# Kernel tuning notes

Measured on AMD Instinct MI355X. Metric: run time of the kernel, lower is better.

## Reference

```python
import jax, jax.numpy as jnp
import numpy as np

B, T, H, LD = 32, 2048, 1024, 1024

def setup_inputs() -> dict:
    key = jax.random.key(0)
    k1, k2, k3, k4, k5 = jax.random.split(key, 5)
    scale = 1.0 / np.sqrt(H)
    return {
        "encoder_hidden": jax.random.normal(k1, (B, T, H), dtype=jnp.float32),
        "decoder_hidden": jax.random.normal(k2, (B, H), dtype=jnp.float32),
        "W1": jax.random.normal(k3, (H, LD), dtype=jnp.float32) * scale,
        "b1": jnp.zeros((LD,), dtype=jnp.float32),
        "W2": jax.random.normal(k4, (H, LD), dtype=jnp.float32) * scale,
        "b2": jnp.zeros((LD,), dtype=jnp.float32),
        "V": jax.random.normal(k5, (LD, 1), dtype=jnp.float32) * (1.0 / np.sqrt(LD)),
        "bV": jnp.zeros((1,), dtype=jnp.float32),
    }

def reference(encoder_hidden, decoder_hidden, W1, b1, W2, b2, V, bV):
    # dec proj: [B, 1, ld]
    dec_w = (decoder_hidden @ W1 + b1)[:, None, :]
    # enc proj: [B, T, ld]
    enc_w = jnp.einsum('bth,hl->btl', encoder_hidden, W2) + b2
    # multiplicative combine (as in source: decoder_Weight * encoder_weight)
    score = jnp.tanh(dec_w * enc_w) @ V + bV          # [B, T, 1]
    attn = jax.nn.softmax(score, axis=1)              # softmax over time
    context = jnp.sum(attn * encoder_hidden, axis=1)  # [B, H]
    return context, attn
```

## Files before the change

kernel.cpp:

```cpp
#include <hip/hip_runtime.h>
#include <hip/hip_bf16.h>
#include <math.h>

#define B_  32
#define T_  2048
#define H_  1024
#define LD_ 1024
#define M_  (B_*T_)

typedef __attribute__((ext_vector_type(8))) short bf16x8;
typedef __attribute__((ext_vector_type(4))) float f32x4;

__device__ __forceinline__ void async_copy16(void* lds, const void* g) {
  __builtin_amdgcn_global_load_lds(
      (const __attribute__((address_space(1))) void*)g,
      (__attribute__((address_space(3))) void*)lds, 16, 0, 0);
}

__global__ void convert_w2(const float* __restrict__ W2, __hip_bfloat16* __restrict__ w2p) {
  int idx = blockIdx.x * 256 + threadIdx.x;
  int kg = idx >> 10, n = idx & 1023;
  __align__(16) __hip_bfloat16 h[8];
#pragma unroll
  for (int j = 0; j < 8; ++j)
    h[j] = __float2bfloat16(W2[(size_t)(kg * 8 + j) * LD_ + n]);
  *reinterpret_cast<uint4*>(&w2p[(size_t)kg * (LD_ * 8) + n * 8]) =
      *reinterpret_cast<const uint4*>(h);
}

__global__ void dec_proj(const float* __restrict__ dec, const float* __restrict__ W1,
                         const float* __restrict__ b1, float* __restrict__ dec_w) {
  __shared__ float sdec[H_];
  int bb = blockIdx.x >> 2;
  int l = (blockIdx.x & 3) * 256 + threadIdx.x;
  for (int i = threadIdx.x; i < H_; i += 256) sdec[i] = dec[bb * H_ + i];
  __syncthreads();
  float a0 = 0.f, a1 = 0.f, a2 = 0.f, a3 = 0.f;
  for (int h = 0; h < H_; h += 4) {
    a0 += sdec[h + 0] * W1[(h + 0) * LD_ + l];
    a1 += sdec[h + 1] * W1[(h + 1) * LD_ + l];
    a2 += sdec[h + 2] * W1[(h + 2) * LD_ + l];
    a3 += sdec[h + 3] * W1[(h + 3) * LD_ + l];
  }
  dec_w[bb * LD_ + l] = (a0 + a1) + (a2 + a3) + b1[l];
}

__global__ __launch_bounds__(256, 2)
void score_gemm(const float* __restrict__ enc,
                const __hip_bfloat16* __restrict__ w2p,
                const float* __restrict__ dec_w,
                const float* __restrict__ b2,
                const float* __restrict__ V,
                float* __restrict__ score) {
  __shared__ __align__(16) __hip_bfloat16 Asm[2][4][128][8];
  __shared__ __align__(16) __hip_bfloat16 Bsm[2][4][256][8];

  const int tid  = threadIdx.x;
  const int lane = tid & 63;
  const int wave = tid >> 6;
  const int wm = wave >> 1, wn = wave & 1;
  const int bid = blockIdx.y * gridDim.x + blockIdx.x;
  const int swz = (bid & 7) * 256 + (bid >> 3);
  const int mb = swz >> 2, nb = swz & 3;
  const int row0 = mb * 128, col0 = nb * 256;
  const int q = lane >> 4, c15 = lane & 15;

  f32x4 acc[4][8] = {};

  const int sm  = tid >> 2;
  const int skg = tid & 3;
  const int sx  = skg * 2;

  const size_t arow0 = (size_t)(row0 + sm) * H_ + skg * 8;
  const size_t arow1 = (size_t)(row0 + 64 + sm) * H_ + skg * 8;

  float4 pf[4];

  auto LOADA = [&](int k0) {
    pf[0] = *reinterpret_cast<const float4*>(enc + arow0 + k0);
    pf[1] = *reinterpret_cast<const float4*>(enc + arow0 + k0 + 4);
    pf[2] = *reinterpret_cast<const float4*>(enc + arow1 + k0);
    pf[3] = *reinterpret_cast<const float4*>(enc + arow1 + k0 + 4);
  };
  auto CVTW = [&](int buf) {
    __align__(16) __hip_bfloat16 h[8];
    h[0] = __float2bfloat16(pf[0].x); h[1] = __float2bfloat16(pf[0].y);
    h[2] = __float2bfloat16(pf[0].z); h[3] = __float2bfloat16(pf[0].w);
    h[4] = __float2bfloat16(pf[1].x); h[5] = __float2bfloat16(pf[1].y);
    h[6] = __float2bfloat16(pf[1].z); h[7] = __float2bfloat16(pf[1].w);
    *reinterpret_cast<uint4*>(&Asm[buf][skg][sm ^ sx][0]) =
        *reinterpret_cast<const uint4*>(h);
    h[0] = __float2bfloat16(pf[2].x); h[1] = __float2bfloat16(pf[2].y);
    h[2] = __float2bfloat16(pf[2].z); h[3] = __float2bfloat16(pf[2].w);
    h[4] = __float2bfloat16(pf[3].x); h[5] = __float2bfloat16(pf[3].y);
    h[6] = __float2bfloat16(pf[3].z); h[7] = __float2bfloat16(pf[3].w);
    *reinterpret_cast<uint4*>(&Asm[buf][skg][(64 + sm) ^ sx][0]) =
        *reinterpret_cast<const uint4*>(h);
  };
  auto GLOADB = [&](int buf, int k0) {
    char* bbase = (char*)&Bsm[buf][0][0][0] + tid * 16;
    const char* gbase = (const char*)w2p + ((size_t)(k0 >> 3)) * (LD_ * 8 * 2)
                        + (size_t)col0 * 16 + tid * 16;
#pragma unroll
    for (int p = 0; p < 4; ++p)
      async_copy16(bbase + p * 4096, gbase + (size_t)p * (LD_ * 8 * 2));
  };

  LOADA(0);
  GLOADB(0, 0);
  CVTW(0);
  __syncthreads();

  for (int t = 0; t < 32; ++t) {
    const int cur = t & 1;
    if (t < 31) {
      LOADA((t + 1) * 32);
      GLOADB(cur ^ 1, (t + 1) * 32);
    }
    bf16x8 af[4], bfr[8];
#pragma unroll
    for (int i = 0; i < 4; ++i)
      af[i] = *reinterpret_cast<const bf16x8*>(
          &Asm[cur][q][(wm * 64 + i * 16 + c15) ^ (q * 2)][0]);
#pragma unroll
    for (int j = 0; j < 8; ++j)
      bfr[j] = *reinterpret_cast<const bf16x8*>(
          &Bsm[cur][q][wn * 128 + j * 16 + c15][0]);
#pragma unroll
    for (int i = 0; i < 4; ++i)
#pragma unroll
      for (int j = 0; j < 8; ++j)
        acc[i][j] = __builtin_amdgcn_mfma_f32_16x16x32_bf16(af[i], bfr[j], acc[i][j], 0, 0, 0);
    if (t < 31) CVTW(cur ^ 1);
    __syncthreads();
  }

  const int bb = row0 >> 11;
  float b2v[8], dwv[8], Vv[8];
#pragma unroll
  for (int j = 0; j < 8; ++j) {
    int n = col0 + wn * 128 + j * 16 + c15;
    b2v[j] = b2[n];
    dwv[j] = dec_w[bb * LD_ + n];
    Vv[j]  = V[n];
  }
#pragma unroll
  for (int i = 0; i < 4; ++i) {
#pragma unroll
    for (int r = 0; r < 4; ++r) {
      float v = 0.f;
#pragma unroll
      for (int j = 0; j < 8; ++j) {
        float e = acc[i][j][r] + b2v[j];
        v += tanhf(dwv[j] * e) * Vv[j];
      }
      v += __shfl_xor(v, 1);
      v += __shfl_xor(v, 2);
      v += __shfl_xor(v, 4);
      v += __shfl_xor(v, 8);
      if (c15 == 0) {
        int row = row0 + wm * 64 + i * 16 + q * 4 + r;
        atomicAdd(&score[row], v);
      }
    }
  }
}

__global__ void softmax_k(const float* __restrict__ score, float* __restrict__ attn) {
  int bb = blockIdx.x;
  int tid = threadIdx.x;
  int lane = tid & 63, wave = tid >> 6;
  __shared__ float red[4];
  float v[8];
  float mx = -3.4e38f;
#pragma unroll
  for (int i = 0; i < 8; ++i) {
    v[i] = score[bb * T_ + i * 256 + tid];
    mx = fmaxf(mx, v[i]);
  }
#pragma unroll
  for (int m = 32; m >= 1; m >>= 1) mx = fmaxf(mx, __shfl_xor(mx, m));
  if (lane == 0) red[wave] = mx;
  __syncthreads();
  mx = fmaxf(fmaxf(red[0], red[1]), fmaxf(red[2], red[3]));
  __syncthreads();
  float s = 0.f;
#pragma unroll
  for (int i = 0; i < 8; ++i) { v[i] = __expf(v[i] - mx); s += v[i]; }
#pragma unroll
  for (int m = 32; m >= 1; m >>= 1) s += __shfl_xor(s, m);
  if (lane == 0) red[wave] = s;
  __syncthreads();
  s = red[0] + red[1] + red[2] + red[3];
  float inv = 1.f / s;
#pragma unroll
  for (int i = 0; i < 8; ++i) attn[bb * T_ + i * 256 + tid] = v[i] * inv;
}

__global__ __launch_bounds__(256)
void context_k(const float* __restrict__ enc, const float* __restrict__ attn,
               float* __restrict__ ctx) {
  const int bb = blockIdx.y;
  const int t0 = blockIdx.x * 128;
  __shared__ float sat[128];
  if (threadIdx.x < 128) sat[threadIdx.x] = attn[bb * T_ + t0 + threadIdx.x];
  __syncthreads();
  const float4* base = reinterpret_cast<const float4*>(
      enc + ((size_t)bb * T_ + t0) * H_) + threadIdx.x;
  f32x4 a0 = {}, a1 = {}, a2 = {}, a3 = {};
  for (int t = 0; t < 128; t += 8) {
    float4 v[8];
#pragma unroll
    for (int u = 0; u < 8; ++u) v[u] = base[(size_t)(t + u) * (H_ / 4)];
#pragma unroll
    for (int u = 0; u < 8; ++u) {
      float a = sat[t + u];
      f32x4& d = (u & 2) ? ((u & 1) ? a3 : a2) : ((u & 1) ? a1 : a0);
      d[0] += a * v[u].x; d[1] += a * v[u].y;
      d[2] += a * v[u].z; d[3] += a * v[u].w;
    }
  }
  const int h = threadIdx.x * 4;
  atomicAdd(&ctx[bb * H_ + h + 0], (a0[0] + a1[0]) + (a2[0] + a3[0]));
  atomicAdd(&ctx[bb * H_ + h + 1], (a0[1] + a1[1]) + (a2[1] + a3[1]));
  atomicAdd(&ctx[bb * H_ + h + 2], (a0[2] + a1[2]) + (a2[2] + a3[2]));
  atomicAdd(&ctx[bb * H_ + h + 3], (a0[3] + a1[3]) + (a2[3] + a3[3]));
}

extern "C" void kernel_launch(void* const* d_in, const int* in_sizes, int n_in,
                              void* d_out, int out_size, void* d_ws, size_t ws_size,
                              hipStream_t stream) {
  const float* enc = (const float*)d_in[0];
  const float* dec = (const float*)d_in[1];
  const float* W1  = (const float*)d_in[2];
  const float* b1  = (const float*)d_in[3];
  const float* W2  = (const float*)d_in[4];
  const float* b2  = (const float*)d_in[5];
  const float* V   = (const float*)d_in[6];

  char* ws = (char*)d_ws;
  __hip_bfloat16* w2p = (__hip_bfloat16*)ws;
  float* dec_w = (float*)(ws + (2u << 20));
  float* score = (float*)(ws + (2u << 20) + (128u << 10));

  float* out  = (float*)d_out;
  float* ctx  = out;
  float* attn = out + B_ * H_;

  hipMemsetAsync(score, 0, (size_t)M_ * sizeof(float), stream);
  hipMemsetAsync(ctx, 0, (size_t)B_ * H_ * sizeof(float), stream);

  convert_w2<<<(H_ * LD_ / 8) / 256, 256, 0, stream>>>(W2, w2p);
  dec_proj<<<B_ * 4, 256, 0, stream>>>(dec, W1, b1, dec_w);
  score_gemm<<<dim3(LD_ / 256, M_ / 128), 256, 0, stream>>>(enc, w2p, dec_w, b2, V, score);
  softmax_k<<<B_, 256, 0, stream>>>(score, attn);
  context_k<<<dim3(16, B_), 256, 0, stream>>>(enc, attn, ctx);
}
```

Measured before the change: 699.3 us.

## Load encoder A fragments directly into registers, drop A LDS staging, double K-step

Each wave now loads its own fp32 encoder rows straight from global memory into registers in MFMA fragment layout and converts them to bf16 in registers, so the shared-memory A tile and its stores are removed. The K loop is unrolled to 64 per iteration with two MFMA phases, and the B tile in LDS is doubled to match, which halves the number of barriers. The cost is that the two wn waves each load the same A rows from global memory (duplicate traffic that relies on cache), register pressure rises, and the wider LDS B buffer may limit occupancy.

```diff
diff --git a/kernel.cpp b/kernel.cpp
--- a/kernel.cpp
+++ b/kernel.cpp
@@ -52,8 +52,7 @@
                 const float* __restrict__ b2,
                 const float* __restrict__ V,
                 float* __restrict__ score) {
-  __shared__ __align__(16) __hip_bfloat16 Asm[2][4][128][8];
-  __shared__ __align__(16) __hip_bfloat16 Bsm[2][4][256][8];
+  __shared__ __align__(16) __hip_bfloat16 Bsm[2][8][256][8];
 
   const int tid  = threadIdx.x;
   const int lane = tid & 63;
@@ -67,71 +66,70 @@
 
   f32x4 acc[4][8] = {};
 
-  const int sm  = tid >> 2;
-  const int skg = tid & 3;
-  const int sx  = skg * 2;
-
-  const size_t arow0 = (size_t)(row0 + sm) * H_ + skg * 8;
-  const size_t arow1 = (size_t)(row0 + 64 + sm) * H_ + skg * 8;
-
-  float4 pf[4];
-
-  auto LOADA = [&](int k0) {
-    pf[0] = *reinterpret_cast<const float4*>(enc + arow0 + k0);
-    pf[1] = *reinterpret_cast<const float4*>(enc + arow0 + k0 + 4);
-    pf[2] = *reinterpret_cast<const float4*>(enc + arow1 + k0);
-    pf[3] = *reinterpret_cast<const float4*>(enc + arow1 + k0 + 4);
+  const float* abase = enc + (size_t)(row0 + wm * 64 + c15) * H_ + q * 8;
+
+  float4 ap[4][2];
+
+  auto ALOAD = [&](int k0) {
+#pragma unroll
+    for (int i = 0; i < 4; ++i) {
+      const float4* s = reinterpret_cast<const float4*>(abase + (size_t)i * 16 * H_ + k0);
+      ap[i][0] = s[0];
+      ap[i][1] = s[1];
+    }
   };
-  auto CVTW = [&](int buf) {
-    __align__(16) __hip_bfloat16 h[8];
-    h[0] = __float2bfloat16(pf[0].x); h[1] = __float2bfloat16(pf[0].y);
-    h[2] = __float2bfloat16(pf[0].z); h[3] = __float2bfloat16(pf[0].w);
-    h[4] = __float2bfloat16(pf[1].x); h[5] = __float2bfloat16(pf[1].y);
-    h[6] = __float2bfloat16(pf[1].z); h[7] = __float2bfloat16(pf[1].w);
-    *reinterpret_cast<uint4*>(&Asm[buf][skg][sm ^ sx][0]) =
-        *reinterpret_cast<const uint4*>(h);
-    h[0] = __float2bfloat16(pf[2].x); h[1] = __float2bfloat16(pf[2].y);
-    h[2] = __float2bfloat16(pf[2].z); h[3] = __float2bfloat16(pf[2].w);
-    h[4] = __float2bfloat16(pf[3].x); h[5] = __float2bfloat16(pf[3].y);
-    h[6] = __float2bfloat16(pf[3].z); h[7] = __float2bfloat16(pf[3].w);
-    *reinterpret_cast<uint4*>(&Asm[buf][skg][(64 + sm) ^ sx][0]) =
-        *reinterpret_cast<const uint4*>(h);
+  auto ACVT = [&](bf16x8* af) {
+#pragma unroll
+    for (int i = 0; i < 4; ++i) {
+      __align__(16) __hip_bfloat16 h[8];
+      h[0] = __float2bfloat16(ap[i][0].x); h[1] = __float2bfloat16(ap[i][0].y);
+      h[2] = __float2bfloat16(ap[i][0].z); h[3] = __float2bfloat16(ap[i][0].w);
+      h[4] = __float2bfloat16(ap[i][1].x); h[5] = __float2bfloat16(ap[i][1].y);
+      h[6] = __float2bfloat16(ap[i][1].z); h[7] = __float2bfloat16(ap[i][1].w);
+      af[i] = *reinterpret_cast<const bf16x8*>(h);
+    }
   };
   auto GLOADB = [&](int buf, int k0) {
     char* bbase = (char*)&Bsm[buf][0][0][0] + tid * 16;
     const char* gbase = (const char*)w2p + ((size_t)(k0 >> 3)) * (LD_ * 8 * 2)
                         + (size_t)col0 * 16 + tid * 16;
 #pragma unroll
-    for (int p = 0; p < 4; ++p)
+    for (int p = 0; p < 8; ++p)
       async_copy16(bbase + p * 4096, gbase + (size_t)p * (LD_ * 8 * 2));
   };
 
-  LOADA(0);
   GLOADB(0, 0);
-  CVTW(0);
-  __syncthreads();
-
-  for (int t = 0; t < 32; ++t) {
+  ALOAD(0);
+  __syncthreads();
+
+  for (int t = 0; t < 16; ++t) {
     const int cur = t & 1;
-    if (t < 31) {
-      LOADA((t + 1) * 32);
-      GLOADB(cur ^ 1, (t + 1) * 32);
-    }
+    const int k0 = t * 64;
     bf16x8 af[4], bfr[8];
-#pragma unroll
-    for (int i = 0; i < 4; ++i)
-      af[i] = *reinterpret_cast<const bf16x8*>(
-          &Asm[cur][q][(wm * 64 + i * 16 + c15) ^ (q * 2)][0]);
+
+    ACVT(af);
+    ALOAD(k0 + 32);
+    if (t < 15) GLOADB(cur ^ 1, k0 + 64);
 #pragma unroll
     for (int j = 0; j < 8; ++j)
-      bfr[j] = *reinterpret_cast<const bf16x8*>(
-          &Bsm[cur][q][wn * 128 + j * 16 + c15][0]);
+      bfr[j] = *reinterpret_cast<const bf16x8*>(&Bsm[cur][q][wn * 128 + j * 16 + c15][0]);
 #pragma unroll
     for (int i = 0; i < 4; ++i)
 #pragma unroll
       for (int j = 0; j < 8; ++j)
         acc[i][j] = __builtin_amdgcn_mfma_f32_16x16x32_bf16(af[i], bfr[j], acc[i][j], 0, 0, 0);
-    if (t < 31) CVTW(cur ^ 1);
+
+    ACVT(af);
+    if (t < 15) ALOAD(k0 + 64);
+#pragma unroll
+    for (int j = 0; j < 8; ++j)
+      bfr[j] = *reinterpret_cast<const bf16x8*>(&Bsm[cur][q + 4][wn * 128 + j * 16 + c15][0]);
+#pragma unroll
+    for (int i = 0; i < 4; ++i)
+#pragma unroll
+      for (int j = 0; j < 8; ++j)
+        acc[i][j] = __builtin_amdgcn_mfma_f32_16x16x32_bf16(af[i], bfr[j], acc[i][j], 0, 0, 0);
+
     __syncthreads();
   }
 
```

Result: slower. 720.6 us (+3.0%).
